# Kernel optimization log

Measured on AMD Instinct MI355X. Metric: run time of the kernel, lower is better.

Reference implementation:

```python
import jax, jax.numpy as jnp
import numpy as np

N_NODES = 50000
N_EDGES = 800000
D_IN = 64
D_OUT = 64

def setup_inputs() -> dict:
    key = jax.random.key(0)
    k1, k2, k3, k4 = jax.random.split(key, 4)
    x = jax.random.normal(k1, (N_NODES, D_IN), dtype=jnp.float32)
    # Linear(in, out, bias=False): weight shape [out, in], Kaiming-uniform-ish scale
    bound = 1.0 / np.sqrt(D_IN)
    W = jax.random.uniform(k2, (D_OUT, D_IN), dtype=jnp.float32, minval=-bound, maxval=bound)
    src = jax.random.randint(k3, (N_EDGES,), 0, N_NODES, dtype=jnp.int32)
    dst = jax.random.randint(k4, (N_EDGES,), 0, N_NODES, dtype=jnp.int32)
    return {"x": x, "W": W, "src": src, "dst": dst}

def reference(x, W, src, dst):
    # update_all(copy_src, sum): for each edge (s, d), add x[s] into node d
    agg = jax.ops.segment_sum(x[src], dst, num_segments=N_NODES)  # [N, D_IN]
    # linear1 (bias=False); dropout is identity at inference
    h = jnp.einsum('nd,od->no', agg, W)  # [N, D_OUT]
    h = jax.nn.relu(h)
    # is_normalize=False -> skip L2 normalize; residual adds input node features
    return h + x
```

## Files before the change

kernel.cpp:

```cpp
#include <hip/hip_runtime.h>

#define D 64
#define NCHUNK 256
#define CAP 48

__device__ __forceinline__ float bflo(unsigned u) { return __uint_as_float(u << 16); }
__device__ __forceinline__ float bfhi(unsigned u) { return __uint_as_float(u & 0xffff0000u); }
__device__ __forceinline__ unsigned short f2bf(float f) {
    unsigned b = __float_as_uint(f);
    return (unsigned short)((b + 0x7fffu + ((b >> 16) & 1u)) >> 16);
}

__device__ __forceinline__ void gemm_body(
    int grp, int tid, float4* lds4, const float* __restrict__ x,
    const float* __restrict__ W, unsigned short* __restrict__ ybf, int n_nodes) {
    float4* As4 = lds4;
    float4* Wc4 = lds4 + 2048;
    const float4* W4 = (const float4*)W;
    for (int i = tid; i < 1024; i += 512) {
        const int kc = i >> 6, o = i & 63;
        Wc4[i] = W4[o * 16 + kc];
    }
    const int base = grp * 128;
    const float4* x4 = (const float4*)x;
#pragma unroll
    for (int r = 0; r < 4; ++r) {
        const int i = r * 512 + tid;
        const int row = i >> 4, col = i & 15;
        const int gidx = base * 16 + i;
        if (gidx < n_nodes * 16) As4[row * 16 + (col ^ (row & 15))] = x4[gidx];
    }
    __syncthreads();
    const int q = tid & 15, g = tid >> 4;
    float acc[4][4];
#pragma unroll
    for (int j = 0; j < 4; ++j)
#pragma unroll
        for (int i = 0; i < 4; ++i) acc[j][i] = 0.f;
    for (int kc = 0; kc < 16; ++kc) {
        float4 a[4], wv[4];
#pragma unroll
        for (int j = 0; j < 4; ++j) {
            const int rr = g * 4 + j;
            a[j] = As4[rr * 16 + (kc ^ (rr & 15))];
        }
#pragma unroll
        for (int i = 0; i < 4; ++i) wv[i] = Wc4[kc * 64 + q + 16 * i];
#pragma unroll
        for (int j = 0; j < 4; ++j)
#pragma unroll
            for (int i = 0; i < 4; ++i) {
                acc[j][i] = fmaf(a[j].x, wv[i].x, acc[j][i]);
                acc[j][i] = fmaf(a[j].y, wv[i].y, acc[j][i]);
                acc[j][i] = fmaf(a[j].z, wv[i].z, acc[j][i]);
                acc[j][i] = fmaf(a[j].w, wv[i].w, acc[j][i]);
            }
    }
#pragma unroll
    for (int j = 0; j < 4; ++j) {
        const int n = base + g * 4 + j;
        if (n >= n_nodes) break;
#pragma unroll
        for (int i = 0; i < 4; ++i)
            ybf[(size_t)n * D + q + 16 * i] = f2bf(acc[j][i]);
    }
}

__global__ __launch_bounds__(512) void hist_gemm_kernel(
    const int* __restrict__ dst, unsigned int* __restrict__ bh32,
    const float* __restrict__ x, const float* __restrict__ W,
    unsigned short* __restrict__ ybf, int n_nodes, int ne) {
    __shared__ float4 lds4[3136];
    const int tid = threadIdx.x;
    if ((int)blockIdx.x < NCHUNK) {
        unsigned int* lds = (unsigned int*)lds4;
        const int nw = (n_nodes + 3) >> 2;
        const int c = blockIdx.x;
        const int csz = (ne + NCHUNK - 1) / NCHUNK;
        const int e0 = c * csz, e1 = min(e0 + csz, ne);
        for (int i = tid; i < nw; i += 512) lds[i] = 0;
        __syncthreads();
        for (int e = e0 + tid; e < e1; e += 512) {
            const int d = dst[e];
            atomicAdd(&lds[d >> 2], 1u << ((d & 3) * 8));
        }
        __syncthreads();
        unsigned int* bh = bh32 + (size_t)c * nw;
        for (int i = tid; i < nw; i += 512) bh[i] = lds[i];
        return;
    }
    gemm_body((int)blockIdx.x - NCHUNK, tid, lds4, x, W, ybf, n_nodes);
}

__global__ __launch_bounds__(512) void colscan_gemm_kernel(
    const float* __restrict__ x, const float* __restrict__ W,
    unsigned char* __restrict__ bh8, int* __restrict__ counts,
    unsigned short* __restrict__ ybf, int n_nodes, int ne, int csb, int grpoff) {
    __shared__ float4 lds4[3136];
    const int tid = threadIdx.x;
    if ((int)blockIdx.x < csb) {
        const int d = blockIdx.x * 512 + tid;
        if (d >= n_nodes) return;
        const size_t npad4 = (size_t)((n_nodes + 3) >> 2) * 4;
        int acc = 0;
        for (int c0 = 0; c0 < NCHUNK; c0 += 8) {
            unsigned char v[8];
#pragma unroll
            for (int k = 0; k < 8; ++k) v[k] = bh8[(size_t)(c0 + k) * npad4 + d];
#pragma unroll
            for (int k = 0; k < 8; ++k) {
                bh8[(size_t)(c0 + k) * npad4 + d] = (unsigned char)acc;
                acc += v[k];
            }
        }
        counts[d] = acc;
        return;
    }
    gemm_body(grpoff + (int)blockIdx.x - csb, tid, lds4, x, W, ybf, n_nodes);
}

__global__ __launch_bounds__(512) void place_kernel(
    const int* __restrict__ src, const int* __restrict__ dst,
    const unsigned int* __restrict__ bh32, int* __restrict__ esrc,
    int n_nodes, int ne) {
    __shared__ unsigned int lw[12544];
    const int c = blockIdx.x;
    const int csz = (ne + NCHUNK - 1) / NCHUNK;
    const int e0 = c * csz, e1 = min(e0 + csz, ne);
    const int nw = (n_nodes + 3) >> 2;
    const unsigned int* bh = bh32 + (size_t)c * nw;
    for (int i = threadIdx.x; i < nw; i += 512) lw[i] = bh[i];
    __syncthreads();
    for (int e = e0 + threadIdx.x; e < e1; e += 512) {
        const int d = dst[e];
        const unsigned old = atomicAdd(&lw[d >> 2], 1u << ((d & 3) * 8));
        const int slot = (old >> ((d & 3) * 8)) & 0xff;
        if (slot < CAP) esrc[d * CAP + slot] = src[e];
    }
}

__global__ void gather_kernel(const int* __restrict__ counts, const int* __restrict__ esrc,
                              const unsigned short* __restrict__ ybf,
                              const float* __restrict__ x, float* __restrict__ out,
                              int n_nodes) {
    const int tid = threadIdx.x;
    const int w = tid >> 6, lane = tid & 63;
    const int g = lane >> 3, m = lane & 7;
    const uint4* Y4 = (const uint4*)ybf;
    const float4* x4 = (const float4*)x;
    float4* out4 = (float4*)out;
    const int nWaves = gridDim.x * 4;

    int n = blockIdx.x * 4 + w;
    int c = 0, s_all = 0;
    if (n < n_nodes) {
        c = min(counts[n], CAP);
        s_all = (lane < c) ? esrc[n * CAP + lane] : 0;
    }
    while (n < n_nodes) {
        const int n2 = n + nWaves;
        int c2 = 0, s2 = 0;
        if (n2 < n_nodes) {
            c2 = min(counts[n2], CAP);
            s2 = (lane < c2) ? esrc[n2 * CAP + lane] : 0;
        }
        float acc[8] = {0.f, 0.f, 0.f, 0.f, 0.f, 0.f, 0.f, 0.f};
        for (int j = 0; j < c; j += 8) {
            const int e = j + g;
            const int s = __shfl(s_all, e);
            if (e < c) {
                const uint4 v = Y4[(size_t)s * 8 + m];
                acc[0] += bflo(v.x); acc[1] += bfhi(v.x);
                acc[2] += bflo(v.y); acc[3] += bfhi(v.y);
                acc[4] += bflo(v.z); acc[5] += bfhi(v.z);
                acc[6] += bflo(v.w); acc[7] += bfhi(v.w);
            }
        }
#pragma unroll
        for (int k = 0; k < 8; ++k) {
            acc[k] += __shfl_xor(acc[k], 8);
            acc[k] += __shfl_xor(acc[k], 16);
            acc[k] += __shfl_xor(acc[k], 32);
        }
        if (lane < 8) {
            const float4 xa = x4[(size_t)n * 16 + lane * 2];
            const float4 xb = x4[(size_t)n * 16 + lane * 2 + 1];
            float4 oa, ob;
            oa.x = fmaxf(acc[0], 0.f) + xa.x;
            oa.y = fmaxf(acc[1], 0.f) + xa.y;
            oa.z = fmaxf(acc[2], 0.f) + xa.z;
            oa.w = fmaxf(acc[3], 0.f) + xa.w;
            ob.x = fmaxf(acc[4], 0.f) + xb.x;
            ob.y = fmaxf(acc[5], 0.f) + xb.y;
            ob.z = fmaxf(acc[6], 0.f) + xb.z;
            ob.w = fmaxf(acc[7], 0.f) + xb.w;
            out4[(size_t)n * 16 + lane * 2] = oa;
            out4[(size_t)n * 16 + lane * 2 + 1] = ob;
        }
        n = n2; c = c2; s_all = s2;
    }
}

extern "C" void kernel_launch(void* const* d_in, const int* in_sizes, int n_in,
                              void* d_out, int out_size, void* d_ws, size_t ws_size,
                              hipStream_t stream) {
    const float* x = (const float*)d_in[0];
    const float* W = (const float*)d_in[1];
    const int* src = (const int*)d_in[2];
    const int* dst = (const int*)d_in[3];
    float* out = (float*)d_out;

    const int n_nodes = in_sizes[0] / D;
    const int n_edges = in_sizes[2];
    const int nw = (n_nodes + 3) >> 2;

    unsigned int* bh32 = (unsigned int*)d_ws;
    int* counts = (int*)(bh32 + (size_t)NCHUNK * nw);
    int* esrc = counts + n_nodes;
    unsigned short* ybf = (unsigned short*)(esrc + (size_t)n_nodes * CAP);

    const int ngrp = (n_nodes + 127) / 128;
    const int g1 = (ngrp + 1) / 2;
    const int g2 = ngrp - g1;
    const int csb = (n_nodes + 511) / 512;

    hist_gemm_kernel<<<NCHUNK + g1, 512, 0, stream>>>(
        dst, bh32, x, W, ybf, n_nodes, n_edges);
    colscan_gemm_kernel<<<csb + g2, 512, 0, stream>>>(
        x, W, (unsigned char*)bh32, counts, ybf, n_nodes, n_edges, csb, g1);
    place_kernel<<<NCHUNK, 512, 0, stream>>>(src, dst, bh32, esrc, n_nodes, n_edges);
    gather_kernel<<<2048, 256, 0, stream>>>(counts, esrc, ybf, x, out, n_nodes);
}
```

Measured before the change: 132.2 us.

## Vectorize edge loads in hist/place, deepen colscan unroll, gather two nodes per wave

The histogram and place kernels now read dst/src as int4, with the chunk size rounded to a multiple of 4 for alignment, and copy LDS to and from global memory as uint4. The column scan unrolls 32 chunks per iteration instead of 8, keeping more byte loads in flight. The gather kernel gives each wave two nodes at once, with two edges per lane group and prefetch two iterations ahead, to raise memory-level parallelism on the random bf16 row gathers. The costs are higher register pressure and some divergence when the two nodes have different edge counts.

```diff
diff --git a/kernel.cpp b/kernel.cpp
--- a/kernel.cpp
+++ b/kernel.cpp
@@ -9,6 +9,9 @@
 __device__ __forceinline__ unsigned short f2bf(float f) {
     unsigned b = __float_as_uint(f);
     return (unsigned short)((b + 0x7fffu + ((b >> 16) & 1u)) >> 16);
+}
+__device__ __forceinline__ int chunk_sz(int ne) {
+    return (((ne + NCHUNK - 1) / NCHUNK) + 3) & ~3;
 }
 
 __device__ __forceinline__ void gemm_body(
@@ -74,19 +77,31 @@
     const int tid = threadIdx.x;
     if ((int)blockIdx.x < NCHUNK) {
         unsigned int* lds = (unsigned int*)lds4;
+        uint4* l4 = (uint4*)lds4;
         const int nw = (n_nodes + 3) >> 2;
         const int c = blockIdx.x;
-        const int csz = (ne + NCHUNK - 1) / NCHUNK;
+        const int csz = chunk_sz(ne);
         const int e0 = c * csz, e1 = min(e0 + csz, ne);
-        for (int i = tid; i < nw; i += 512) lds[i] = 0;
+        const int len = max(0, e1 - e0), len4 = len >> 2;
+        for (int i = tid; i < 3136; i += 512) l4[i] = make_uint4(0u, 0u, 0u, 0u);
         __syncthreads();
-        for (int e = e0 + tid; e < e1; e += 512) {
+        const int4* d4 = (const int4*)(dst + e0);
+        for (int i = tid; i < len4; i += 512) {
+            const int4 dd = d4[i];
+            atomicAdd(&lds[dd.x >> 2], 1u << ((dd.x & 3) * 8));
+            atomicAdd(&lds[dd.y >> 2], 1u << ((dd.y & 3) * 8));
+            atomicAdd(&lds[dd.z >> 2], 1u << ((dd.z & 3) * 8));
+            atomicAdd(&lds[dd.w >> 2], 1u << ((dd.w & 3) * 8));
+        }
+        for (int e = e0 + (len & ~3) + tid; e < e1; e += 512) {
             const int d = dst[e];
             atomicAdd(&lds[d >> 2], 1u << ((d & 3) * 8));
         }
         __syncthreads();
         unsigned int* bh = bh32 + (size_t)c * nw;
-        for (int i = tid; i < nw; i += 512) bh[i] = lds[i];
+        uint4* bh4 = (uint4*)bh;
+        for (int i = tid; i < (nw >> 2); i += 512) bh4[i] = l4[i];
+        for (int i = (nw & ~3) + tid; i < nw; i += 512) bh[i] = lds[i];
         return;
     }
     gemm_body((int)blockIdx.x - NCHUNK, tid, lds4, x, W, ybf, n_nodes);
@@ -103,12 +118,12 @@
         if (d >= n_nodes) return;
         const size_t npad4 = (size_t)((n_nodes + 3) >> 2) * 4;
         int acc = 0;
-        for (int c0 = 0; c0 < NCHUNK; c0 += 8) {
-            unsigned char v[8];
-#pragma unroll
-            for (int k = 0; k < 8; ++k) v[k] = bh8[(size_t)(c0 + k) * npad4 + d];
-#pragma unroll
-            for (int k = 0; k < 8; ++k) {
+        for (int c0 = 0; c0 < NCHUNK; c0 += 32) {
+            unsigned char v[32];
+#pragma unroll
+            for (int k = 0; k < 32; ++k) v[k] = bh8[(size_t)(c0 + k) * npad4 + d];
+#pragma unroll
+            for (int k = 0; k < 32; ++k) {
                 bh8[(size_t)(c0 + k) * npad4 + d] = (unsigned char)acc;
                 acc += v[k];
             }
@@ -125,13 +140,31 @@
     int n_nodes, int ne) {
     __shared__ unsigned int lw[12544];
     const int c = blockIdx.x;
-    const int csz = (ne + NCHUNK - 1) / NCHUNK;
+    const int csz = chunk_sz(ne);
     const int e0 = c * csz, e1 = min(e0 + csz, ne);
+    const int len = max(0, e1 - e0), len4 = len >> 2;
     const int nw = (n_nodes + 3) >> 2;
     const unsigned int* bh = bh32 + (size_t)c * nw;
-    for (int i = threadIdx.x; i < nw; i += 512) lw[i] = bh[i];
+    uint4* lw4 = (uint4*)lw;
+    const uint4* bh4 = (const uint4*)bh;
+    for (int i = threadIdx.x; i < (nw >> 2); i += 512) lw4[i] = bh4[i];
+    for (int i = (nw & ~3) + threadIdx.x; i < nw; i += 512) lw[i] = bh[i];
     __syncthreads();
-    for (int e = e0 + threadIdx.x; e < e1; e += 512) {
+    const int4* d4 = (const int4*)(dst + e0);
+    const int4* s4 = (const int4*)(src + e0);
+    for (int i = threadIdx.x; i < len4; i += 512) {
+        const int4 dd = d4[i];
+        const int4 ss = s4[i];
+#pragma unroll
+        for (int k = 0; k < 4; ++k) {
+            const int d = (k == 0) ? dd.x : (k == 1) ? dd.y : (k == 2) ? dd.z : dd.w;
+            const int s = (k == 0) ? ss.x : (k == 1) ? ss.y : (k == 2) ? ss.z : ss.w;
+            const unsigned old = atomicAdd(&lw[d >> 2], 1u << ((d & 3) * 8));
+            const int slot = (old >> ((d & 3) * 8)) & 0xff;
+            if (slot < CAP) esrc[d * CAP + slot] = s;
+        }
+    }
+    for (int e = e0 + (len & ~3) + threadIdx.x; e < e1; e += 512) {
         const int d = dst[e];
         const unsigned old = atomicAdd(&lw[d >> 2], 1u << ((d & 3) * 8));
         const int slot = (old >> ((d & 3) * 8)) & 0xff;
@@ -149,55 +182,106 @@
     const uint4* Y4 = (const uint4*)ybf;
     const float4* x4 = (const float4*)x;
     float4* out4 = (float4*)out;
-    const int nWaves = gridDim.x * 4;
-
-    int n = blockIdx.x * 4 + w;
-    int c = 0, s_all = 0;
-    if (n < n_nodes) {
-        c = min(counts[n], CAP);
-        s_all = (lane < c) ? esrc[n * CAP + lane] : 0;
-    }
-    while (n < n_nodes) {
-        const int n2 = n + nWaves;
-        int c2 = 0, s2 = 0;
-        if (n2 < n_nodes) {
-            c2 = min(counts[n2], CAP);
-            s2 = (lane < c2) ? esrc[n2 * CAP + lane] : 0;
-        }
-        float acc[8] = {0.f, 0.f, 0.f, 0.f, 0.f, 0.f, 0.f, 0.f};
-        for (int j = 0; j < c; j += 8) {
-            const int e = j + g;
-            const int s = __shfl(s_all, e);
-            if (e < c) {
-                const uint4 v = Y4[(size_t)s * 8 + m];
-                acc[0] += bflo(v.x); acc[1] += bfhi(v.x);
-                acc[2] += bflo(v.y); acc[3] += bfhi(v.y);
-                acc[4] += bflo(v.z); acc[5] += bfhi(v.z);
-                acc[6] += bflo(v.w); acc[7] += bfhi(v.w);
+    const int S = gridDim.x * 4;
+
+    int n0 = blockIdx.x * 4 + w;
+    int c0 = 0, s0 = 0, c1 = 0, s1 = 0;
+    if (n0 < n_nodes) {
+        c0 = min(counts[n0], CAP);
+        s0 = (lane < c0) ? esrc[n0 * CAP + lane] : 0;
+    }
+    if (n0 + S < n_nodes) {
+        c1 = min(counts[n0 + S], CAP);
+        s1 = (lane < c1) ? esrc[(n0 + S) * CAP + lane] : 0;
+    }
+    while (n0 < n_nodes) {
+        const int n1 = n0 + S;
+        const int np0 = n0 + 2 * S, np1 = n0 + 3 * S;
+        int pc0 = 0, ps0 = 0, pc1 = 0, ps1 = 0;
+        if (np0 < n_nodes) {
+            pc0 = min(counts[np0], CAP);
+            ps0 = (lane < pc0) ? esrc[np0 * CAP + lane] : 0;
+        }
+        if (np1 < n_nodes) {
+            pc1 = min(counts[np1], CAP);
+            ps1 = (lane < pc1) ? esrc[np1 * CAP + lane] : 0;
+        }
+        float a0[8] = {0.f, 0.f, 0.f, 0.f, 0.f, 0.f, 0.f, 0.f};
+        float a1[8] = {0.f, 0.f, 0.f, 0.f, 0.f, 0.f, 0.f, 0.f};
+        const int cmax = max(c0, c1);
+        for (int j = 0; j < cmax; j += 16) {
+            const int e0 = j + g * 2, e1 = e0 + 1;
+            const int sa0 = __shfl(s0, e0), sb0 = __shfl(s0, e1);
+            const int sa1 = __shfl(s1, e0), sb1 = __shfl(s1, e1);
+            if (e0 < c0) {
+                const uint4 v = Y4[(size_t)sa0 * 8 + m];
+                a0[0] += bflo(v.x); a0[1] += bfhi(v.x);
+                a0[2] += bflo(v.y); a0[3] += bfhi(v.y);
+                a0[4] += bflo(v.z); a0[5] += bfhi(v.z);
+                a0[6] += bflo(v.w); a0[7] += bfhi(v.w);
+            }
+            if (e1 < c0) {
+                const uint4 v = Y4[(size_t)sb0 * 8 + m];
+                a0[0] += bflo(v.x); a0[1] += bfhi(v.x);
+                a0[2] += bflo(v.y); a0[3] += bfhi(v.y);
+                a0[4] += bflo(v.z); a0[5] += bfhi(v.z);
+                a0[6] += bflo(v.w); a0[7] += bfhi(v.w);
+            }
+            if (e0 < c1) {
+                const uint4 v = Y4[(size_t)sa1 * 8 + m];
+                a1[0] += bflo(v.x); a1[1] += bfhi(v.x);
+                a1[2] += bflo(v.y); a1[3] += bfhi(v.y);
+                a1[4] += bflo(v.z); a1[5] += bfhi(v.z);
+                a1[6] += bflo(v.w); a1[7] += bfhi(v.w);
+            }
+            if (e1 < c1) {
+                const uint4 v = Y4[(size_t)sb1 * 8 + m];
+                a1[0] += bflo(v.x); a1[1] += bfhi(v.x);
+                a1[2] += bflo(v.y); a1[3] += bfhi(v.y);
+                a1[4] += bflo(v.z); a1[5] += bfhi(v.z);
+                a1[6] += bflo(v.w); a1[7] += bfhi(v.w);
             }
         }
 #pragma unroll
         for (int k = 0; k < 8; ++k) {
-            acc[k] += __shfl_xor(acc[k], 8);
-            acc[k] += __shfl_xor(acc[k], 16);
-            acc[k] += __shfl_xor(acc[k], 32);
+            a0[k] += __shfl_xor(a0[k], 8);
+            a1[k] += __shfl_xor(a1[k], 8);
+            a0[k] += __shfl_xor(a0[k], 16);
+            a1[k] += __shfl_xor(a1[k], 16);
+            a0[k] += __shfl_xor(a0[k], 32);
+            a1[k] += __shfl_xor(a1[k], 32);
         }
         if (lane < 8) {
-            const float4 xa = x4[(size_t)n * 16 + lane * 2];
-            const float4 xb = x4[(size_t)n * 16 + lane * 2 + 1];
+            const float4 xa = x4[(size_t)n0 * 16 + lane * 2];
+            const float4 xb = x4[(size_t)n0 * 16 + lane * 2 + 1];
             float4 oa, ob;
-            oa.x = fmaxf(acc[0], 0.f) + xa.x;
-            oa.y = fmaxf(acc[1], 0.f) + xa.y;
-            oa.z = fmaxf(acc[2], 0.f) + xa.z;
-            oa.w = fmaxf(acc[3], 0.f) + xa.w;
-            ob.x = fmaxf(acc[4], 0.f) + xb.x;
-            ob.y = fmaxf(acc[5], 0.f) + xb.y;
-            ob.z = fmaxf(acc[6], 0.f) + xb.z;
-            ob.w = fmaxf(acc[7], 0.f) + xb.w;
-            out4[(size_t)n * 16 + lane * 2] = oa;
-            out4[(size_t)n * 16 + lane * 2 + 1] = ob;
-        }
-        n = n2; c = c2; s_all = s2;
+            oa.x = fmaxf(a0[0], 0.f) + xa.x;
+            oa.y = fmaxf(a0[1], 0.f) + xa.y;
+            oa.z = fmaxf(a0[2], 0.f) + xa.z;
+            oa.w = fmaxf(a0[3], 0.f) + xa.w;
+            ob.x = fmaxf(a0[4], 0.f) + xb.x;
+            ob.y = fmaxf(a0[5], 0.f) + xb.y;
+            ob.z = fmaxf(a0[6], 0.f) + xb.z;
+            ob.w = fmaxf(a0[7], 0.f) + xb.w;
+            out4[(size_t)n0 * 16 + lane * 2] = oa;
+            out4[(size_t)n0 * 16 + lane * 2 + 1] = ob;
+        }
+        if (n1 < n_nodes && lane < 8) {
+            const float4 xa = x4[(size_t)n1 * 16 + lane * 2];
+            const float4 xb = x4[(size_t)n1 * 16 + lane * 2 + 1];
+            float4 oa, ob;
+            oa.x = fmaxf(a1[0], 0.f) + xa.x;
+            oa.y = fmaxf(a1[1], 0.f) + xa.y;
+            oa.z = fmaxf(a1[2], 0.f) + xa.z;
+            oa.w = fmaxf(a1[3], 0.f) + xa.w;
+            ob.x = fmaxf(a1[4], 0.f) + xb.x;
+            ob.y = fmaxf(a1[5], 0.f) + xb.y;
+            ob.z = fmaxf(a1[6], 0.f) + xb.z;
+            ob.w = fmaxf(a1[7], 0.f) + xb.w;
+            out4[(size_t)n1 * 16 + lane * 2] = oa;
+            out4[(size_t)n1 * 16 + lane * 2 + 1] = ob;
+        }
+        n0 += 2 * S; c0 = pc0; s0 = ps0; c1 = pc1; s1 = ps1;
     }
 }
 
```

Result: no change. 130.8 us (-1.1%).
